# Kernel tuning notes

Hardware: AMD Instinct MI355X
Metric: run time of the kernel (lower is better)

The kernel has to match this reference:

```python
import jax, jax.numpy as jnp
import numpy as np

HEADS = 16
DHEAD = 128
B, S, DMODEL = 2, 2048, 2048


def setup_inputs() -> dict:
    key = jax.random.key(0)
    k1, k2, k3 = jax.random.split(key, 3)
    x = jax.random.normal(k1, (B, S, DMODEL), dtype=jnp.float32)
    # Linear weights, stored as [in, out] so forward is x @ w (no bias).
    w_in = jax.random.normal(k2, (DMODEL, 3 * HEADS * DHEAD), dtype=jnp.float32) * (DMODEL ** -0.5)
    w_out = jax.random.normal(k3, (HEADS * DHEAD, DMODEL), dtype=jnp.float32) * ((HEADS * DHEAD) ** -0.5)
    # Causal mask: True = masked (strictly upper triangular), broadcast over batch & heads.
    mask = jnp.triu(jnp.ones((S, S), dtype=jnp.bool_), k=1)[None, None, :, :]
    return {"x": x, "w_in": w_in, "w_out": w_out, "mask": mask}


def reference(x, w_in, w_out, mask):
    b, s, _ = x.shape
    # Fused QKV projection: [b,s,3*H*dh] -> [b,s,H,3*dh] -> chunk into q,k,v [b,s,H,dh]
    projected = (x @ w_in).reshape(b, s, HEADS, 3 * DHEAD)
    q, k, v = jnp.split(projected, 3, axis=-1)
    # Scores [b,H,l,L], scaled by 1/sqrt(dhead)
    scale = 1.0 / (DHEAD ** 0.5)
    a = jnp.einsum("blhd,bLhd->bhlL", q, k) * scale
    a = jnp.where(mask, -jnp.inf, a)
    a = jax.nn.softmax(a, axis=-1)
    # Weighted values -> [b,l,H,dh] -> flatten heads -> output projection
    out = jnp.einsum("bhlL,bLhd->blhd", a, v).reshape(b, s, HEADS * DHEAD)
    return out @ w_out
```

## Files before the change

kernel.cpp:

```cpp
#include <hip/hip_runtime.h>

#define HD    16
#define DH    128
#define BB    2
#define SS    2048
#define DM    2048
#define NQKV  6144
#define MTOT  4096

typedef short   bfx8  __attribute__((ext_vector_type(8)));
typedef float   f32x4 __attribute__((ext_vector_type(4)));

__device__ __forceinline__ unsigned short f2bf(float f) {
  union { float f; unsigned int u; } c; c.f = f;
  unsigned int u = c.u + 0x7FFFu + ((c.u >> 16) & 1u);
  return (unsigned short)(u >> 16);
}

__device__ __forceinline__ void gload_lds16(const unsigned short* g, unsigned short* l) {
  __builtin_amdgcn_global_load_lds(
      (const __attribute__((address_space(1))) unsigned int*)g,
      (__attribute__((address_space(3))) unsigned int*)l, 16, 0, 0);
}

#define BARS() do { __builtin_amdgcn_sched_barrier(0); __builtin_amdgcn_s_barrier(); \
                    __builtin_amdgcn_sched_barrier(0); } while (0)
#define VMCNT8() do { asm volatile("s_waitcnt vmcnt(8)" ::: "memory"); \
                      __builtin_amdgcn_sched_barrier(0); } while (0)

__global__ __launch_bounds__(256) void f32_to_bf16_k(const float* __restrict__ in,
                                                     unsigned short* __restrict__ out, int n4) {
  int i = (blockIdx.x * 256 + threadIdx.x);
  if (i >= n4) return;
  const float4 v = *(const float4*)(in + (size_t)i * 4);
  ushort4 o;
  o.x = f2bf(v.x); o.y = f2bf(v.y); o.z = f2bf(v.z); o.w = f2bf(v.w);
  *(ushort4*)(out + (size_t)i * 4) = o;
}

__global__ __launch_bounds__(256) void transpose_f32_bf16_k(const float* __restrict__ in,
                                                            unsigned short* __restrict__ out,
                                                            int R, int C) {
  __shared__ float t[32][33];
  const int c0 = blockIdx.x * 32, r0 = blockIdx.y * 32;
  const int tx = threadIdx.x & 31, ty = threadIdx.x >> 5;
#pragma unroll
  for (int i = 0; i < 4; i++) {
    int r = r0 + ty + i * 8;
    t[ty + i * 8][tx] = in[(size_t)r * C + c0 + tx];
  }
  __syncthreads();
#pragma unroll
  for (int i = 0; i < 4; i++) {
    int c = c0 + ty + i * 8;
    out[(size_t)c * R + r0 + tx] = f2bf(t[tx][ty + i * 8]);
  }
}

__global__ __launch_bounds__(512, 2) void gemm256_qkv_k(const unsigned short* __restrict__ A,
                                                        const unsigned short* __restrict__ Bt,
                                                        unsigned short* __restrict__ Qg,
                                                        unsigned short* __restrict__ Kg,
                                                        unsigned short* __restrict__ Vg,
                                                        int K) {
  __shared__ __align__(16) unsigned short Asb[2][256 * 64];
  __shared__ __align__(16) unsigned short Bsb[2][256 * 64];
  const int tid = threadIdx.x;
  const int lane = tid & 63, wid = tid >> 6;
  const int wr = wid >> 2, wc = wid & 3;
  const int cbase = lane & 15, rgrp = lane >> 4;
  const int bid = (int)blockIdx.x;
  const int id = (bid & 7) * 48 + (bid >> 3);
  const int nb = id >> 4, mb = id & 15;
  const size_t m0 = (size_t)mb * 256, n0 = (size_t)nb * 256;
  const int nkt = K >> 6;

#define STAGE_HALF(u_, half_) do {                                                      \
    const int uc_ = ((u_) < nkt ? (u_) : (nkt - 1));                                    \
    unsigned short* ldsb_ = (((half_) < 2) ? &Asb[(u_) & 1][0] : &Bsb[(u_) & 1][0])     \
                            + ((half_) & 1) * (128 * 64);                               \
    const unsigned short* gb_ = (((half_) < 2)                                          \
        ? A  + (m0 + (size_t)((half_) & 1) * 128) * (size_t)K                           \
        : Bt + (n0 + (size_t)((half_) & 1) * 128) * (size_t)K);                         \
    _Pragma("unroll")                                                                   \
    for (int ld_ = 0; ld_ < 2; ld_++) {                                                 \
      const int idx_ = ld_ * 512 + tid;                                                 \
      const int row_ = idx_ >> 3, seg_ = idx_ & 7;                                      \
      gload_lds16(gb_ + (size_t)row_ * K + uc_ * 64 +                                   \
                      (((seg_ * 16) ^ ((row_ & 7) << 4)) >> 1),                         \
                  ldsb_ + idx_ * 8);                                                    \
    } } while (0)

  const int axor = (cbase & 7) << 4;
  int a_off[2], b_off[2];
#pragma unroll
  for (int ks = 0; ks < 2; ks++) {
    a_off[ks] = ((wr * 128 + cbase) * 128 + ((ks * 64 + rgrp * 16) ^ axor)) >> 1;
    b_off[ks] = ((wc * 64 + cbase) * 128 + ((ks * 64 + rgrp * 16) ^ axor)) >> 1;
  }

  f32x4 acc[8][4];
  const f32x4 z = {0.f, 0.f, 0.f, 0.f};
#pragma unroll
  for (int mf = 0; mf < 8; mf++)
#pragma unroll
    for (int nf = 0; nf < 4; nf++) acc[mf][nf] = z;

  STAGE_HALF(0, 2); STAGE_HALF(0, 3); STAGE_HALF(0, 0); STAGE_HALF(0, 1);
  STAGE_HALF(1, 2); STAGE_HALF(1, 3); STAGE_HALF(1, 0); STAGE_HALF(1, 1);
  VMCNT8();
  BARS();

#pragma unroll 1
  for (int u = 0; u < nkt; ++u) {
    const unsigned short* As_ = &Asb[u & 1][0];
    const unsigned short* Bs_ = &Bsb[u & 1][0];
    bfx8 a03[4][2], a47[4][2], b01[2][2], b23[2][2];

#pragma unroll
    for (int mf = 0; mf < 4; mf++)
#pragma unroll
      for (int ks = 0; ks < 2; ks++)
        a03[mf][ks] = *(const bfx8*)(As_ + a_off[ks] + mf * 1024);
#pragma unroll
    for (int nf = 0; nf < 2; nf++)
#pragma unroll
      for (int ks = 0; ks < 2; ks++)
        b01[nf][ks] = *(const bfx8*)(Bs_ + b_off[ks] + nf * 1024);
    BARS();
    __builtin_amdgcn_s_setprio(1);
#pragma unroll
    for (int mf = 0; mf < 4; mf++)
#pragma unroll
      for (int nf = 0; nf < 2; nf++)
#pragma unroll
        for (int ks = 0; ks < 2; ks++)
          acc[mf][nf] = __builtin_amdgcn_mfma_f32_16x16x32_bf16(a03[mf][ks], b01[nf][ks], acc[mf][nf], 0, 0, 0);
    __builtin_amdgcn_s_setprio(0);
    BARS();

#pragma unroll
    for (int nf = 0; nf < 2; nf++)
#pragma unroll
      for (int ks = 0; ks < 2; ks++)
        b23[nf][ks] = *(const bfx8*)(Bs_ + b_off[ks] + (nf + 2) * 1024);
    BARS();
    __builtin_amdgcn_s_setprio(1);
#pragma unroll
    for (int mf = 0; mf < 4; mf++)
#pragma unroll
      for (int nf = 0; nf < 2; nf++)
#pragma unroll
        for (int ks = 0; ks < 2; ks++)
          acc[mf][nf + 2] = __builtin_amdgcn_mfma_f32_16x16x32_bf16(a03[mf][ks], b23[nf][ks], acc[mf][nf + 2], 0, 0, 0);
    __builtin_amdgcn_s_setprio(0);
    BARS();

#pragma unroll
    for (int mf = 0; mf < 4; mf++)
#pragma unroll
      for (int ks = 0; ks < 2; ks++)
        a47[mf][ks] = *(const bfx8*)(As_ + a_off[ks] + (mf + 4) * 1024);
    STAGE_HALF(u + 2, 2);
    STAGE_HALF(u + 2, 3);
    BARS();
    __builtin_amdgcn_s_setprio(1);
#pragma unroll
    for (int mf = 0; mf < 4; mf++)
#pragma unroll
      for (int nf = 0; nf < 2; nf++)
#pragma unroll
        for (int ks = 0; ks < 2; ks++)
          acc[mf + 4][nf] = __builtin_amdgcn_mfma_f32_16x16x32_bf16(a47[mf][ks], b01[nf][ks], acc[mf + 4][nf], 0, 0, 0);
    __builtin_amdgcn_s_setprio(0);
    BARS();

    STAGE_HALF(u + 2, 0);
    STAGE_HALF(u + 2, 1);
    VMCNT8();
    BARS();
    __builtin_amdgcn_s_setprio(1);
#pragma unroll
    for (int mf = 0; mf < 4; mf++)
#pragma unroll
      for (int nf = 0; nf < 2; nf++)
#pragma unroll
        for (int ks = 0; ks < 2; ks++)
          acc[mf + 4][nf + 2] = __builtin_amdgcn_mfma_f32_16x16x32_bf16(a47[mf][ks], b23[nf][ks], acc[mf + 4][nf + 2], 0, 0, 0);
    __builtin_amdgcn_s_setprio(0);
    BARS();
  }
#undef STAGE_HALF

#pragma unroll
  for (int mf = 0; mf < 8; mf++)
#pragma unroll
    for (int nf = 0; nf < 4; nf++) {
      const int nn = (int)n0 + wc * 64 + nf * 16;
      const int h = nn / 384, tt = (nn >> 7) % 3;
      const int d = (nn & 127) + cbase;
      const int row0 = (int)m0 + wr * 128 + mf * 16 + rgrp * 4;
      const int bb = row0 >> 11;
      const int s0 = row0 & 2047;
      if (tt == 2) {
        ushort4 v;
        v.x = f2bf(acc[mf][nf][0]); v.y = f2bf(acc[mf][nf][1]);
        v.z = f2bf(acc[mf][nf][2]); v.w = f2bf(acc[mf][nf][3]);
        *(ushort4*)(Vg + ((size_t)(bb * HD + h) * DH + d) * SS + s0) = v;
      } else {
        unsigned short* dst = (tt == 0 ? Qg : Kg);
#pragma unroll
        for (int r = 0; r < 4; r++)
          dst[((size_t)(bb * HD + h) * SS + s0 + r) * DH + d] = f2bf(acc[mf][nf][r]);
      }
    }
}

__global__ __launch_bounds__(256) void gemm_out_k(const unsigned short* __restrict__ A,
                                                  const unsigned short* __restrict__ Bt,
                                                  float* __restrict__ C, int K, int ldc) {
  __shared__ __align__(16) unsigned short As[128 * 32];
  __shared__ __align__(16) unsigned short Bs[128 * 32];
  const int tid = threadIdx.x;
  const int lane = tid & 63, wid = tid >> 6;
  const int wr = wid >> 1, wc = wid & 1;
  const int cbase = lane & 15, rgrp = lane >> 4;
  const size_t m0 = (size_t)blockIdx.y * 128, n0 = (size_t)blockIdx.x * 128;

  f32x4 acc[4][4];
  const f32x4 z = {0.f, 0.f, 0.f, 0.f};
#pragma unroll
  for (int mf = 0; mf < 4; mf++)
#pragma unroll
    for (int nf = 0; nf < 4; nf++) acc[mf][nf] = z;

  const int nkt = K >> 5;
  for (int kt = 0; kt < nkt; ++kt) {
#pragma unroll
    for (int i = 0; i < 2; i++) {
      int idx = i * 256 + tid;
      int row = idx >> 2, cb = idx & 3;
      gload_lds16(A + (m0 + row) * K + (kt * 32 + cb * 8), As + idx * 8);
      gload_lds16(Bt + (n0 + row) * K + (kt * 32 + cb * 8), Bs + idx * 8);
    }
    __syncthreads();
    bfx8 af[4], bfr[4];
#pragma unroll
    for (int mf = 0; mf < 4; mf++)
      af[mf] = *(const bfx8*)(As + (wr * 64 + mf * 16 + cbase) * 32 + rgrp * 8);
#pragma unroll
    for (int nf = 0; nf < 4; nf++)
      bfr[nf] = *(const bfx8*)(Bs + (wc * 64 + nf * 16 + cbase) * 32 + rgrp * 8);
#pragma unroll
    for (int mf = 0; mf < 4; mf++)
#pragma unroll
      for (int nf = 0; nf < 4; nf++)
        acc[mf][nf] = __builtin_amdgcn_mfma_f32_16x16x32_bf16(af[mf], bfr[nf], acc[mf][nf], 0, 0, 0);
    __syncthreads();
  }

#pragma unroll
  for (int mf = 0; mf < 4; mf++)
#pragma unroll
    for (int nf = 0; nf < 4; nf++)
#pragma unroll
      for (int r = 0; r < 4; r++) {
        size_t row = m0 + wr * 64 + mf * 16 + rgrp * 4 + r;
        size_t col = n0 + wc * 64 + nf * 16 + cbase;
        C[row * ldc + col] = acc[mf][nf][r];
      }
}

__global__ __launch_bounds__(256) void attn_fwd_k(const unsigned short* __restrict__ Qg,
                                                  const unsigned short* __restrict__ Kg,
                                                  const unsigned short* __restrict__ Vg,
                                                  unsigned short* __restrict__ ao) {
  __shared__ __align__(16) unsigned short Klds[2][64 * 128];
  __shared__ __align__(16) unsigned short Vt[2][128 * 64];
  __shared__ __align__(16) unsigned short Plds[4][16 * 64];
  const int tid = threadIdx.x;
  const int lane = tid & 63, wid = tid >> 6;
  const int cbase = lane & 15, rgrp = lane >> 4;
  const int cx = (cbase & 7) << 4;

  const int bid = (int)blockIdx.x;
  const int bh = (bid & 7) * 4 + ((bid >> 3) & 3);
  const int qt = 31 - (bid >> 5);
  const int b = bh >> 4, h = bh & 15;
  const int qbase = qt * 64;

  const unsigned short* qp0 = Qg + (size_t)(b * HD + h) * SS * DH;
  const unsigned short* kp  = Kg + (size_t)(b * HD + h) * SS * DH;
  const unsigned short* vp  = Vg + (size_t)(b * HD + h) * DH * SS;
  const float scale = 0.08838834764831845f;
  const f32x4 z = {0.f, 0.f, 0.f, 0.f};
  const int qi = qbase + wid * 16 + cbase;

  bfx8 qf[4];
  {
    const unsigned short* qp = qp0 + (size_t)qi * DH;
#pragma unroll
    for (int ks = 0; ks < 4; ks++) qf[ks] = *(const bfx8*)(qp + ks * 32 + rgrp * 8);
  }

  float m_run = -1e30f, l_run = 0.f;
  f32x4 o[8];
#pragma unroll
  for (int mb = 0; mb < 8; mb++) o[mb] = z;

#define STAGE_T(t_, s_) do {                                                        \
    const int kvb_ = (t_) * 64;                                                     \
    _Pragma("unroll")                                                               \
    for (int i_ = 0; i_ < 4; i_++) {                                                \
      int idx_ = i_ * 256 + tid;                                                    \
      int r_ = idx_ >> 4, bo_ = (idx_ & 15) * 16;                                   \
      gload_lds16(kp + (size_t)(kvb_ + r_) * DH + ((bo_ ^ ((r_ & 7) << 4)) >> 1),   \
                  &Klds[s_][idx_ * 8]);                                             \
    }                                                                               \
    _Pragma("unroll")                                                               \
    for (int i_ = 0; i_ < 4; i_++) {                                                \
      int idx_ = i_ * 256 + tid;                                                    \
      int d_ = idx_ >> 3, bo_ = (idx_ & 7) * 16;                                    \
      gload_lds16(vp + (size_t)d_ * SS + kvb_ + ((bo_ ^ ((d_ & 7) << 4)) >> 1),     \
                  &Vt[s_][idx_ * 8]);                                               \
    } } while (0)

  const int ntiles = qt + 1;
  STAGE_T(0, 0);
  __syncthreads();

  for (int t = 0; t < ntiles; ++t) {
    const int sel = t & 1;
    if (t + 1 < ntiles) STAGE_T(t + 1, sel ^ 1);
    const unsigned short* Ks_ = &Klds[sel][0];
    const unsigned short* Vs_ = &Vt[sel][0];
    const int kvb = t * 64;

    f32x4 s[4];
#pragma unroll
    for (int mf = 0; mf < 4; mf++) s[mf] = z;
#pragma unroll
    for (int mf = 0; mf < 4; mf++)
#pragma unroll
      for (int ks = 0; ks < 4; ks++) {
        bfx8 kf = *(const bfx8*)(Ks_ + (((mf * 16 + cbase) * 256 + ((ks * 64 + rgrp * 16) ^ cx)) >> 1));
        s[mf] = __builtin_amdgcn_mfma_f32_16x16x32_bf16(kf, qf[ks], s[mf], 0, 0, 0);
      }

    float sv[4][4];
    const bool diag = (t == ntiles - 1);
#pragma unroll
    for (int mf = 0; mf < 4; mf++)
#pragma unroll
      for (int r = 0; r < 4; r++) {
        float v = s[mf][r] * scale;
        if (diag && (kvb + mf * 16 + rgrp * 4 + r > qi)) v = -1e30f;
        sv[mf][r] = v;
      }
    float tm = sv[0][0];
#pragma unroll
    for (int mf = 0; mf < 4; mf++)
#pragma unroll
      for (int r = 0; r < 4; r++) tm = fmaxf(tm, sv[mf][r]);
    tm = fmaxf(tm, __shfl_xor(tm, 16));
    tm = fmaxf(tm, __shfl_xor(tm, 32));
    const float mnew = fmaxf(m_run, tm);
    float p[4][4];
    float rs = 0.f;
#pragma unroll
    for (int mf = 0; mf < 4; mf++)
#pragma unroll
      for (int r = 0; r < 4; r++) { p[mf][r] = __expf(sv[mf][r] - mnew); rs += p[mf][r]; }
    rs += __shfl_xor(rs, 16);
    rs += __shfl_xor(rs, 32);
    const float alpha = __expf(m_run - mnew);
    l_run = l_run * alpha + rs;
    m_run = mnew;
#pragma unroll
    for (int mb = 0; mb < 8; mb++)
#pragma unroll
      for (int r = 0; r < 4; r++) o[mb][r] *= alpha;

#pragma unroll
    for (int mf = 0; mf < 4; mf++)
#pragma unroll
      for (int rr = 0; rr < 2; rr++) {
        unsigned int pp = (unsigned int)f2bf(p[mf][2 * rr]) |
                          ((unsigned int)f2bf(p[mf][2 * rr + 1]) << 16);
        *(unsigned int*)((char*)&Plds[wid][0] +
                         (cbase * 128 + ((mf * 32 + rgrp * 8 + rr * 4) ^ cx))) = pp;
      }
    bfx8 pf[2];
#pragma unroll
    for (int k2 = 0; k2 < 2; k2++)
      pf[k2] = *(const bfx8*)((const char*)&Plds[wid][0] +
                              (cbase * 128 + ((k2 * 64 + rgrp * 16) ^ cx)));

#pragma unroll
    for (int mb = 0; mb < 8; mb++)
#pragma unroll
      for (int k2 = 0; k2 < 2; k2++) {
        bfx8 vf = *(const bfx8*)(Vs_ + (((mb * 16 + cbase) * 128 + ((k2 * 64 + rgrp * 16) ^ cx)) >> 1));
        o[mb] = __builtin_amdgcn_mfma_f32_16x16x32_bf16(vf, pf[k2], o[mb], 0, 0, 0);
      }
    __syncthreads();
  }
#undef STAGE_T

  const float rinv = 1.0f / l_run;
  unsigned short* aop = ao + ((size_t)(b * SS + qi)) * DM + h * DH + rgrp * 4;
#pragma unroll
  for (int mb = 0; mb < 8; mb++) {
    ushort4 v;
    v.x = f2bf(o[mb][0] * rinv); v.y = f2bf(o[mb][1] * rinv);
    v.z = f2bf(o[mb][2] * rinv); v.w = f2bf(o[mb][3] * rinv);
    *(ushort4*)(aop + mb * 16) = v;
  }
}

extern "C" void kernel_launch(void* const* d_in, const int* in_sizes, int n_in,
                              void* d_out, int out_size, void* d_ws, size_t ws_size,
                              hipStream_t stream) {
  (void)in_sizes; (void)n_in; (void)out_size; (void)ws_size;
  const float* x     = (const float*)d_in[0];
  const float* w_in  = (const float*)d_in[1];
  const float* w_out = (const float*)d_in[2];
  float* out = (float*)d_out;

  char* ws = (char*)d_ws;
  unsigned short* Xb  = (unsigned short*)(ws);
  unsigned short* Wit = (unsigned short*)(ws + (16ull << 20));
  unsigned short* Wot = (unsigned short*)(ws + (40ull << 20));
  unsigned short* Qg  = (unsigned short*)(ws + (48ull << 20));
  unsigned short* Kg  = (unsigned short*)(ws + (64ull << 20));
  unsigned short* Vg  = (unsigned short*)(ws + (80ull << 20));
  unsigned short* AO  = (unsigned short*)(ws + (96ull << 20));

  f32_to_bf16_k<<<MTOT * DM / 4 / 256, 256, 0, stream>>>(x, Xb, MTOT * DM / 4);
  transpose_f32_bf16_k<<<dim3(NQKV / 32, DM / 32), 256, 0, stream>>>(w_in, Wit, DM, NQKV);
  transpose_f32_bf16_k<<<dim3(DM / 32, DM / 32), 256, 0, stream>>>(w_out, Wot, DM, DM);
  gemm256_qkv_k<<<384, 512, 0, stream>>>(Xb, Wit, Qg, Kg, Vg, DM);
  attn_fwd_k<<<1024, 256, 0, stream>>>(Qg, Kg, Vg, AO);
  gemm_out_k<<<dim3(DM / 128, MTOT / 128), 256, 0, stream>>>(AO, Wot, out, DM, DM);
}
```

Baseline: 279.3 us.

## Prefetch next k-tile A03/B01 fragments during last MFMA quarter

```diff
diff --git a/kernel.cpp b/kernel.cpp
--- a/kernel.cpp
+++ b/kernel.cpp
@@ -99,6 +99,33 @@
     b_off[ks] = ((wc * 64 + cbase) * 128 + ((ks * 64 + rgrp * 16) ^ axor)) >> 1;
   }
 
+#define RD_A03(dst_, p_) do { _Pragma("unroll")                                          \
+    for (int mf_ = 0; mf_ < 4; mf_++) { _Pragma("unroll")                                \
+      for (int ks_ = 0; ks_ < 2; ks_++)                                                  \
+        dst_[mf_][ks_] = *(const bfx8*)((p_) + a_off[ks_] + mf_ * 1024); } } while (0)
+#define RD_A47(dst_, p_) do { _Pragma("unroll")                                          \
+    for (int mf_ = 0; mf_ < 4; mf_++) { _Pragma("unroll")                                \
+      for (int ks_ = 0; ks_ < 2; ks_++)                                                  \
+        dst_[mf_][ks_] = *(const bfx8*)((p_) + a_off[ks_] + (mf_ + 4) * 1024); } } while (0)
+#define RD_B01(dst_, p_) do { _Pragma("unroll")                                          \
+    for (int nf_ = 0; nf_ < 2; nf_++) { _Pragma("unroll")                                \
+      for (int ks_ = 0; ks_ < 2; ks_++)                                                  \
+        dst_[nf_][ks_] = *(const bfx8*)((p_) + b_off[ks_] + nf_ * 1024); } } while (0)
+#define RD_B23(dst_, p_) do { _Pragma("unroll")                                          \
+    for (int nf_ = 0; nf_ < 2; nf_++) { _Pragma("unroll")                                \
+      for (int ks_ = 0; ks_ < 2; ks_++)                                                  \
+        dst_[nf_][ks_] = *(const bfx8*)((p_) + b_off[ks_] + (nf_ + 2) * 1024); } } while (0)
+
+#define MFMA_Q(mo_, no_, AF_, BF_) do {                                                  \
+    __builtin_amdgcn_s_setprio(1);                                                      \
+    _Pragma("unroll")                                                                    \
+    for (int mf_ = 0; mf_ < 4; mf_++) { _Pragma("unroll")                                \
+      for (int nf_ = 0; nf_ < 2; nf_++) { _Pragma("unroll")                              \
+        for (int ks_ = 0; ks_ < 2; ks_++)                                                \
+          acc[mf_ + (mo_)][nf_ + (no_)] = __builtin_amdgcn_mfma_f32_16x16x32_bf16(       \
+              AF_[mf_][ks_], BF_[nf_][ks_], acc[mf_ + (mo_)][nf_ + (no_)], 0, 0, 0); } } \
+    __builtin_amdgcn_s_setprio(0); } while (0)
+
   f32x4 acc[8][4];
   const f32x4 z = {0.f, 0.f, 0.f, 0.f};
 #pragma unroll
@@ -110,86 +137,48 @@
   STAGE_HALF(1, 2); STAGE_HALF(1, 3); STAGE_HALF(1, 0); STAGE_HALF(1, 1);
   VMCNT8();
   BARS();
+  bfx8 a03A[4][2], b01A[2][2], a03B[4][2], b01B[2][2];
+  RD_A03(a03A, &Asb[0][0]);
+  RD_B01(b01A, &Bsb[0][0]);
+
+#define TILE_BODY(u_, A03_, B01_, NA03_, NB01_) do {                                     \
+    const unsigned short* As_  = &Asb[(u_) & 1][0];                                      \
+    const unsigned short* Bs_  = &Bsb[(u_) & 1][0];                                      \
+    const unsigned short* Asn_ = &Asb[((u_) + 1) & 1][0];                                \
+    const unsigned short* Bsn_ = &Bsb[((u_) + 1) & 1][0];                                \
+    bfx8 a47[4][2], b23[2][2];                                                           \
+                     \
+    RD_B23(b23, Bs_);                                                                    \
+    BARS();                                                                              \
+    MFMA_Q(0, 0, A03_, B01_);                                                            \
+    BARS();                                                 \
+                       \
+    RD_A47(a47, As_);                                                                    \
+    STAGE_HALF((u_) + 2, 2); STAGE_HALF((u_) + 2, 3);                                    \
+    BARS();                                                                              \
+    MFMA_Q(0, 2, A03_, b23);                                                             \
+    BARS();                                                 \
+                                        \
+    STAGE_HALF((u_) + 2, 0); STAGE_HALF((u_) + 2, 1);                                    \
+    BARS();                                                                              \
+    MFMA_Q(4, 0, a47, B01_);                                                             \
+    BARS();                                                                              \
+      \
+                             \
+    VMCNT8();                                                                            \
+    BARS();                                                                              \
+    RD_A03(NA03_, Asn_);                                                                 \
+    RD_B01(NB01_, Bsn_);                                                                 \
+    MFMA_Q(4, 2, a47, b23);                                                              \
+    BARS();                                                                              \
+  } while (0)
 
 #pragma unroll 1
-  for (int u = 0; u < nkt; ++u) {
-    const unsigned short* As_ = &Asb[u & 1][0];
-    const unsigned short* Bs_ = &Bsb[u & 1][0];
-    bfx8 a03[4][2], a47[4][2], b01[2][2], b23[2][2];
-
-#pragma unroll
-    for (int mf = 0; mf < 4; mf++)
-#pragma unroll
-      for (int ks = 0; ks < 2; ks++)
-        a03[mf][ks] = *(const bfx8*)(As_ + a_off[ks] + mf * 1024);
-#pragma unroll
-    for (int nf = 0; nf < 2; nf++)
-#pragma unroll
-      for (int ks = 0; ks < 2; ks++)
-        b01[nf][ks] = *(const bfx8*)(Bs_ + b_off[ks] + nf * 1024);
-    BARS();
-    __builtin_amdgcn_s_setprio(1);
-#pragma unroll
-    for (int mf = 0; mf < 4; mf++)
-#pragma unroll
-      for (int nf = 0; nf < 2; nf++)
-#pragma unroll
-        for (int ks = 0; ks < 2; ks++)
-          acc[mf][nf] = __builtin_amdgcn_mfma_f32_16x16x32_bf16(a03[mf][ks], b01[nf][ks], acc[mf][nf], 0, 0, 0);
-    __builtin_amdgcn_s_setprio(0);
-    BARS();
-
-#pragma unroll
-    for (int nf = 0; nf < 2; nf++)
-#pragma unroll
-      for (int ks = 0; ks < 2; ks++)
-        b23[nf][ks] = *(const bfx8*)(Bs_ + b_off[ks] + (nf + 2) * 1024);
-    BARS();
-    __builtin_amdgcn_s_setprio(1);
-#pragma unroll
-    for (int mf = 0; mf < 4; mf++)
-#pragma unroll
-      for (int nf = 0; nf < 2; nf++)
-#pragma unroll
-        for (int ks = 0; ks < 2; ks++)
-          acc[mf][nf + 2] = __builtin_amdgcn_mfma_f32_16x16x32_bf16(a03[mf][ks], b23[nf][ks], acc[mf][nf + 2], 0, 0, 0);
-    __builtin_amdgcn_s_setprio(0);
-    BARS();
-
-#pragma unroll
-    for (int mf = 0; mf < 4; mf++)
-#pragma unroll
-      for (int ks = 0; ks < 2; ks++)
-        a47[mf][ks] = *(const bfx8*)(As_ + a_off[ks] + (mf + 4) * 1024);
-    STAGE_HALF(u + 2, 2);
-    STAGE_HALF(u + 2, 3);
-    BARS();
-    __builtin_amdgcn_s_setprio(1);
-#pragma unroll
-    for (int mf = 0; mf < 4; mf++)
-#pragma unroll
-      for (int nf = 0; nf < 2; nf++)
-#pragma unroll
-        for (int ks = 0; ks < 2; ks++)
-          acc[mf + 4][nf] = __builtin_amdgcn_mfma_f32_16x16x32_bf16(a47[mf][ks], b01[nf][ks], acc[mf + 4][nf], 0, 0, 0);
-    __builtin_amdgcn_s_setprio(0);
-    BARS();
-
-    STAGE_HALF(u + 2, 0);
-    STAGE_HALF(u + 2, 1);
-    VMCNT8();
-    BARS();
-    __builtin_amdgcn_s_setprio(1);
-#pragma unroll
-    for (int mf = 0; mf < 4; mf++)
-#pragma unroll
-      for (int nf = 0; nf < 2; nf++)
-#pragma unroll
-        for (int ks = 0; ks < 2; ks++)
-          acc[mf + 4][nf + 2] = __builtin_amdgcn_mfma_f32_16x16x32_bf16(a47[mf][ks], b23[nf][ks], acc[mf + 4][nf + 2], 0, 0, 0);
-    __builtin_amdgcn_s_setprio(0);
-    BARS();
-  }
+  for (int u = 0; u < nkt; u += 2) {
+    TILE_BODY(u,     a03A, b01A, a03B, b01B);
+    TILE_BODY(u + 1, a03B, b01B, a03A, b01A);
+  }
+#undef TILE_BODY
 #undef STAGE_HALF
 
 #pragma unroll
```

New measurement: 273.1 us. 1.02x faster.
